# Performance work log

Measured on AMD Instinct MI355X. Metric: run time of the kernel, lower is better.

The kernel has to match this reference:

```python
import jax, jax.numpy as jnp
import numpy as np

B, N, C = 64, 256, 512
SHIFTS = (-1, 0, 1)
# torch.chunk(N, 3): ceil(256/3)=86 -> sizes [86, 86, 84]
CHUNK_SIZES = (86, 86, 84)
EPS = 1e-5


def _shift_pad(a, s):
    # shift along last axis (C) with zero padding, matching shift_with_padding
    if s == 0:
        return a
    if s > 0:
        return jnp.pad(a[..., :-s], ((0, 0), (0, 0), (s, 0)))
    s = -s
    return jnp.pad(a[..., s:], ((0, 0), (0, 0), (0, s)))


def setup_inputs() -> dict:
    key = jax.random.key(0)
    ks = jax.random.split(key, 16)
    w = lambda k, shape: (jax.random.normal(k, shape, jnp.float32) * 0.02)
    inp = {
        "x": jax.random.normal(ks[0], (B, N, C), jnp.float32),
        "ln_g": jnp.ones((C,), jnp.float32),
        "ln_b": jnp.zeros((C,), jnp.float32),
        "Ws": w(ks[1], (C, C)),
        "bs": jnp.zeros((C,), jnp.float32),
        "Wc": w(ks[2], (N, N, 3)),     # Conv1d weight [out=N, in=N, k=3]
        "bc": jnp.zeros((N,), jnp.float32),
        "We1": w(ks[3], (N, N // 8)),
        "be1": jnp.zeros((N // 8,), jnp.float32),
        "We2": w(ks[4], (N // 8, N)),
        "be2": jnp.zeros((N,), jnp.float32),
        "Wf1": w(ks[5], (C, 2 * C)),
        "bf1": jnp.zeros((2 * C,), jnp.float32),
        "Wf2": w(ks[6], (2 * C, C)),
        "bf2": jnp.zeros((C,), jnp.float32),
    }
    return inp


def reference(x, ln_g, ln_b, Ws, bs, Wc, bc, We1, be1, We2, be2, Wf1, bf1, Wf2, bf2):
    res = x
    # channel_mixer_S: LayerNorm over C, then Linear C->C + relu (dropout=0)
    mu = jnp.mean(x, axis=-1, keepdims=True)
    var = jnp.mean((x - mu) ** 2, axis=-1, keepdims=True)
    h = (x - mu) * jax.lax.rsqrt(var + EPS) * ln_g + ln_b
    h = jax.nn.relu(h @ Ws + bs)                      # [B, N, C]
    # channel_shift: chunk along N, shift each chunk along C with zero pad
    offs = np.cumsum((0,) + CHUNK_SIZES)
    chunks = [h[:, offs[i]:offs[i + 1], :] for i in range(3)]
    x_shift = jnp.concatenate([_shift_pad(c, s) for c, s in zip(chunks, SHIFTS)], axis=1)
    # channel_projection: Conv1d over C with N channels, k=3, pad=1
    x_shift = jax.lax.conv_general_dilated(
        x_shift, Wc, window_strides=(1,), padding=[(1, 1)],
        dimension_numbers=("NCH", "OIH", "NCH")) + bc[None, :, None]
    # SE gating
    se = jnp.mean(x_shift, axis=-1)                   # [B, N]
    ex = jax.nn.sigmoid(jax.nn.relu(se @ We1 + be1) @ We2 + be2)  # [B, N]
    z = x_shift * ex[:, :, None]
    # channel_mixer_F: C -> 2C (relu) -> C, residual
    z = jax.nn.relu(z @ Wf1 + bf1) @ Wf2 + bf2 + res
    return z
```

## Files before the change

### kernel.cpp

```cpp
#include <hip/hip_runtime.h>
#include <hip/hip_bf16.h>
#include <math.h>

#define BB 64
#define NN 256
#define CCH 512

typedef unsigned short u16;
typedef __attribute__((ext_vector_type(8))) short s16x8;
typedef __attribute__((ext_vector_type(4))) float f32x4;

#define AS1 __attribute__((address_space(1)))
#define AS3 __attribute__((address_space(3)))

static __device__ __forceinline__ float b2f(u16 u) {
    union { unsigned int i; float f; } x; x.i = ((unsigned int)u) << 16; return x.f;
}
static __device__ __forceinline__ u16 f2b(float f) {
    __hip_bfloat16 h = __float2bfloat16(f);
    union { __hip_bfloat16 h; u16 u; } x; x.h = h; return x.u;
}
static __device__ __forceinline__ void gll16(const void* g, void* l) {
    __builtin_amdgcn_global_load_lds((const AS1 unsigned int*)g,
                                     (AS3 unsigned int*)l, 16, 0, 0);
}

#define VM3  asm volatile("s_waitcnt vmcnt(3)" ::: "memory")
#define VM0  asm volatile("s_waitcnt vmcnt(0)" ::: "memory")
#define MEMB asm volatile("" ::: "memory")

__global__ __launch_bounds__(128) void ln_kernel(const float* __restrict__ x,
    const float* __restrict__ g, const float* __restrict__ bta,
    u16* __restrict__ out)
{
    int r = blockIdx.x;
    const float4* xr = (const float4*)(x + (size_t)r * CCH);
    float4 v = xr[threadIdx.x];
    float s  = v.x + v.y + v.z + v.w;
    float ss = v.x*v.x + v.y*v.y + v.z*v.z + v.w*v.w;
    #pragma unroll
    for (int o = 32; o > 0; o >>= 1) {
        s  += __shfl_down(s, o);
        ss += __shfl_down(ss, o);
    }
    __shared__ float red[4];
    int wid = threadIdx.x >> 6;
    if ((threadIdx.x & 63) == 0) { red[wid] = s; red[2 + wid] = ss; }
    __syncthreads();
    s  = red[0] + red[1];
    ss = red[2] + red[3];
    float mu  = s * (1.0f / CCH);
    float var = ss * (1.0f / CCH) - mu * mu;
    float rs  = rsqrtf(var + 1e-5f);
    float4 gv = ((const float4*)g)[threadIdx.x];
    float4 bv = ((const float4*)bta)[threadIdx.x];
    ushort4 o;
    o.x = f2b((v.x - mu) * rs * gv.x + bv.x);
    o.y = f2b((v.y - mu) * rs * gv.y + bv.y);
    o.z = f2b((v.z - mu) * rs * gv.z + bv.z);
    o.w = f2b((v.w - mu) * rs * gv.w + bv.w);
    ((ushort4*)(out + (size_t)r * CCH))[threadIdx.x] = o;
}

static __device__ __forceinline__ void wtc_body(const float* __restrict__ W,
    u16* __restrict__ Wt, int K, int N, int bx, int by, float* t )
{
    int n0 = bx * 32, k0 = by * 32;
    int tx = threadIdx.x & 31, ty = threadIdx.x >> 5;
    #pragma unroll
    for (int i = 0; i < 4; ++i)
        t[(ty + i * 8) * 33 + tx] = W[(size_t)(k0 + ty + i * 8) * N + n0 + tx];
    __syncthreads();
    #pragma unroll
    for (int i = 0; i < 4; ++i)
        Wt[(size_t)(n0 + ty + i * 8) * K + k0 + tx] = f2b(t[tx * 33 + ty + i * 8]);
}

__global__ __launch_bounds__(256) void prep_kernel(
    const float* __restrict__ Ws,  u16* __restrict__ Wst,
    const float* __restrict__ Wf1, u16* __restrict__ Wf1t,
    const float* __restrict__ Wf2, u16* __restrict__ Wf2t,
    const float* __restrict__ Wc,  u16* __restrict__ Wc3,
    u16* __restrict__ Hts, float* __restrict__ SEraw)
{
    __shared__ float t[32 * 33];
    int bid = blockIdx.x;
    if (bid < 256) {
        wtc_body(Ws, Wst, 512, 512, bid & 15, bid >> 4, t);
    } else if (bid < 768) {
        int idx = bid - 256;
        wtc_body(Wf1, Wf1t, 512, 1024, idx & 31, idx >> 5, t);
    } else if (bid < 1280) {
        int idx = bid - 768;
        wtc_body(Wf2, Wf2t, 1024, 512, idx & 15, idx >> 4, t);
    } else if (bid < 2048) {
        int idx = (bid - 1280) * 256 + threadIdx.x;
        int i = idx & 255;
        int o = (idx >> 8) & 255;
        int k = idx >> 16;
        Wc3[idx] = f2b(Wc[((size_t)o * NN + i) * 3 + k]);
    } else {
        int idx = (bid - 2048) * 256 + threadIdx.x;
        if (idx < 65536) {
            int b   = idx >> 10;
            int rem = idx & 1023;
            int rr  = rem >> 8;
            int r   = (rr & 1) + (rr >> 1) * 512;
            Hts[((size_t)b * 514 + r) * 256 + (rem & 255)] = 0;
        } else {
            SEraw[idx - 65536] = 0.0f;
        }
    }
}

template<int MODE>
__global__ __launch_bounds__(512, 1) void gemm_pipe(
    const u16* __restrict__ A, const u16* __restrict__ Bt,
    const float* __restrict__ bias, const float* __restrict__ scale,
    const float* __restrict__ res, void* __restrict__ outv,
    u16* __restrict__ auxout, float* __restrict__ SEraw)
{
    constexpr int NT = (MODE == 0) ? 8 : (MODE == 1) ? 8 : (MODE == 2) ? 16 : 12;
    constexpr int SA = (MODE == 2) ? 1024 : 512;
    constexpr int SB = (MODE == 2) ? 1024 : 512;
    constexpr int NOUT = (MODE == 1) ? 1024 : 512;

    __shared__ u16 Asm[2 * 2 * 256 * 32];
    __shared__ u16 Bsm[2 * 2 * 128 * 32];

    const int tid = threadIdx.x;
    const int l   = tid & 63;
    const int w   = tid >> 6;
    const int nwg = gridDim.x;
    const int work = (blockIdx.x & 7) * (nwg >> 3) + (blockIdx.x >> 3);

    int row0, col0, bidx = 0;
    if (MODE == 0)      { row0 = (work >> 7) * 256; col0 = (work & 127) * 128; }
    else if (MODE == 1) { row0 = (work >> 3) * 256; col0 = (work & 7) * 128; }
    else if (MODE == 2) { row0 = (work >> 2) * 256; col0 = (work & 3) * 128; }
    else                { row0 = 0; bidx = work >> 2; col0 = (work & 3) * 128; }

    const u16* Aab  = A + (size_t)row0 * SA;
    const u16* Bab  = Bt + (size_t)col0 * SB;
    const u16* HtsB = Bt + (size_t)bidx * 514 * 256;

    const int wm = (w >> 2) * 128;
    const int wn = (w & 3) * 32;
    const int fr = l & 15;
    const int fk = (l >> 4) * 8;

    const f32x4 zero = {0.0f, 0.0f, 0.0f, 0.0f};
    f32x4 acc[8][2];
    #pragma unroll
    for (int m = 0; m < 8; ++m) { acc[m][0] = zero; acc[m][1] = zero; }

    auto stageA = [&](int buf, int t1, int ks) {
        u16* ald = Asm + (buf * 2 + ks) * 8192 + w * 512;
        int s = w * 64 + l;
        if (MODE == 3) {
            const int kseg = t1 >> 2, kb = (t1 & 3) * 64 + ks * 32;
            gll16(A + kseg * 65536 + (s >> 2) * 256 + kb + (s & 3) * 8, ald);
            s += 512;
            gll16(A + kseg * 65536 + (s >> 2) * 256 + kb + (s & 3) * 8, ald + 4096);
        } else {
            const int kb = t1 * 64 + ks * 32;
            gll16(Aab + (size_t)(s >> 2) * SA + kb + (s & 3) * 8, ald);
            s += 512;
            gll16(Aab + (size_t)(s >> 2) * SA + kb + (s & 3) * 8, ald + 4096);
        }
    };
    auto stageB = [&](int buf, int t1, int ks) {
        u16* bld = Bsm + (buf * 2 + ks) * 4096 + w * 512;
        const int s = tid;
        if (MODE == 3) {
            const int kseg = t1 >> 2, kb = (t1 & 3) * 64 + ks * 32;
            gll16(HtsB + (size_t)(col0 + (s >> 2) + kseg) * 256 + kb + (s & 3) * 8, bld);
        } else {
            const int kb = t1 * 64 + ks * 32;
            gll16(Bab + (size_t)(s >> 2) * SB + kb + (s & 3) * 8, bld);
        }
    };

    stageA(0, 0, 0); stageB(0, 0, 0);
    stageA(0, 0, 1); stageB(0, 0, 1);

    int buf = 0;
    for (int t = 0; t < NT; ++t) {
        const bool more = (t + 1 < NT);
        #pragma unroll
        for (int ks = 0; ks < 2; ++ks) {
            if (ks == 0) { VM3; }
            else if (more) { VM3; } else { VM0; }
            __builtin_amdgcn_s_barrier();
            MEMB;
            s16x8 bf0 = *(const s16x8*)&Bsm[(buf * 2 + ks) * 4096 + (wn + 0 * 16 + fr) * 32 + fk];
            s16x8 bf1v = *(const s16x8*)&Bsm[(buf * 2 + ks) * 4096 + (wn + 1 * 16 + fr) * 32 + fk];
            s16x8 af[8];
            #pragma unroll
            for (int m = 0; m < 8; ++m)
                af[m] = *(const s16x8*)&Asm[(buf * 2 + ks) * 8192 + (wm + m * 16 + fr) * 32 + fk];
            if (more) { stageA(buf ^ 1, t + 1, ks); stageB(buf ^ 1, t + 1, ks); }
            __builtin_amdgcn_s_setprio(1);
            #pragma unroll
            for (int m = 0; m < 8; ++m) {
                acc[m][0] = __builtin_amdgcn_mfma_f32_16x16x32_bf16(af[m], bf0,  acc[m][0], 0, 0, 0);
                acc[m][1] = __builtin_amdgcn_mfma_f32_16x16x32_bf16(af[m], bf1v, acc[m][1], 0, 0, 0);
            }
            __builtin_amdgcn_s_setprio(0);
        }
        buf ^= 1;
    }

    if (MODE == 0) {
        #pragma unroll
        for (int m = 0; m < 8; ++m) {
            #pragma unroll
            for (int j = 0; j < 4; ++j) {
                const int c = row0 + wm + m * 16 + (l >> 4) * 4 + j;
                const float bsv = bias[c];
                #pragma unroll
                for (int n = 0; n < 2; ++n) {
                    const int gcol = col0 + wn + n * 16 + fr;
                    const int b  = gcol >> 8;
                    const int ni = gcol & 255;
                    const int s  = (ni < 86) ? -1 : (ni < 172 ? 0 : 1);
                    auxout[((size_t)b * 514 + c + 1 + s) * 256 + ni] =
                        f2b(fmaxf(acc[m][n][j] + bsv, 0.0f));
                }
            }
        }
    } else if (MODE == 1) {
        #pragma unroll
        for (int m = 0; m < 8; ++m) {
            #pragma unroll
            for (int j = 0; j < 4; ++j) {
                const int row = row0 + wm + m * 16 + (l >> 4) * 4 + j;
                const float sc = scale[row];
                #pragma unroll
                for (int n = 0; n < 2; ++n) {
                    const int col = col0 + wn + n * 16 + fr;
                    ((u16*)outv)[(size_t)row * NOUT + col] =
                        f2b(fmaxf(acc[m][n][j] * sc + bias[col], 0.0f));
                }
            }
        }
    } else if (MODE == 2) {
        #pragma unroll
        for (int m = 0; m < 8; ++m) {
            #pragma unroll
            for (int j = 0; j < 4; ++j) {
                const int row = row0 + wm + m * 16 + (l >> 4) * 4 + j;
                #pragma unroll
                for (int n = 0; n < 2; ++n) {
                    const int col = col0 + wn + n * 16 + fr;
                    ((float*)outv)[(size_t)row * NOUT + col] =
                        acc[m][n][j] + bias[col] + res[(size_t)row * NOUT + col];
                }
            }
        }
    } else {
        #pragma unroll
        for (int m = 0; m < 8; ++m) {
            #pragma unroll
            for (int j = 0; j < 4; ++j) {
                const int no = wm + m * 16 + (l >> 4) * 4 + j;
                const float bcv = bias[no];
                float p = 0.0f;
                #pragma unroll
                for (int n = 0; n < 2; ++n) {
                    const int c = col0 + wn + n * 16 + fr;
                    float v = acc[m][n][j];
                    auxout[((size_t)bidx * NN + no) * CCH + c] = f2b(v + bcv);
                    p += v;
                }
                p += __shfl_xor(p, 1);
                p += __shfl_xor(p, 2);
                p += __shfl_xor(p, 4);
                p += __shfl_xor(p, 8);
                if (fr == 0) atomicAdd(&SEraw[bidx * NN + no], p);
            }
        }
    }
}

__global__ __launch_bounds__(256) void semlp_kernel(const float* __restrict__ seraw,
    const float* __restrict__ bc,
    const float* __restrict__ We1, const float* __restrict__ be1,
    const float* __restrict__ We2, const float* __restrict__ be2,
    float* __restrict__ ex)
{
    __shared__ float sse[256];
    __shared__ float e1[32];
    int b = blockIdx.x, t = threadIdx.x;
    sse[t] = seraw[b * 256 + t] * (1.0f / CCH) + bc[t];
    __syncthreads();
    if (t < 32) {
        float a = be1[t];
        #pragma unroll 8
        for (int i = 0; i < 256; ++i) a += sse[i] * We1[i * 32 + t];
        e1[t] = fmaxf(a, 0.0f);
    }
    __syncthreads();
    float a = be2[t];
    #pragma unroll
    for (int j = 0; j < 32; ++j) a += e1[j] * We2[j * 256 + t];
    ex[b * 256 + t] = 1.0f / (1.0f + expf(-a));
}

extern "C" void kernel_launch(void* const* d_in, const int* in_sizes, int n_in,
                              void* d_out, int out_size, void* d_ws, size_t ws_size,
                              hipStream_t stream) {
    const float* x    = (const float*)d_in[0];
    const float* ln_g = (const float*)d_in[1];
    const float* ln_b = (const float*)d_in[2];
    const float* Ws   = (const float*)d_in[3];
    const float* bs   = (const float*)d_in[4];
    const float* Wc   = (const float*)d_in[5];
    const float* bc   = (const float*)d_in[6];
    const float* We1  = (const float*)d_in[7];
    const float* be1  = (const float*)d_in[8];
    const float* We2  = (const float*)d_in[9];
    const float* be2  = (const float*)d_in[10];
    const float* Wf1  = (const float*)d_in[11];
    const float* bf1  = (const float*)d_in[12];
    const float* Wf2  = (const float*)d_in[13];
    const float* bf2  = (const float*)d_in[14];
    float* out = (float*)d_out;
    char* w8   = (char*)d_ws;

    u16* XN  = (u16*)(w8);
    u16* Y   = XN;
    u16* Hts = (u16*)(w8 + (16u << 20));
    u16* T   = (u16*)(w8 + (16u << 20));
    char* tail = w8 + 50397184;
    float* SEraw = (float*)(tail);
    float* EX    = (float*)(tail + 65536);
    u16* Wst     = (u16*)(tail + 131072);
    u16* Wf1t    = (u16*)(tail + 655360);
    u16* Wf2t    = (u16*)(tail + 1703936);
    u16* Wc3     = (u16*)(tail + 2752512);

    prep_kernel<<<2368, 256, 0, stream>>>(Ws, Wst, Wf1, Wf1t, Wf2, Wf2t,
                                          Wc, Wc3, Hts, SEraw);
    ln_kernel<<<BB * NN, 128, 0, stream>>>(x, ln_g, ln_b, XN);
    gemm_pipe<0><<<256, 512, 0, stream>>>(Wst, XN, bs, nullptr, nullptr,
                                          nullptr, Hts, nullptr);
    gemm_pipe<3><<<256, 512, 0, stream>>>(Wc3, Hts, bc, nullptr, nullptr,
                                          nullptr, Y, SEraw);
    semlp_kernel<<<BB, 256, 0, stream>>>(SEraw, bc, We1, be1, We2, be2, EX);
    gemm_pipe<1><<<512, 512, 0, stream>>>(Y, Wf1t, bf1, EX, nullptr,
                                          T, nullptr, nullptr);
    gemm_pipe<2><<<256, 512, 0, stream>>>(T, Wf2t, bf2, nullptr, x,
                                          out, nullptr, nullptr);
}
```

Baseline: 134.7 us.

## Deepen GEMM pipeline to four LDS slots with XOR-swizzled K layout; wave-per-row LayerNorm

The GEMM main loop drops the double-buffered two-half-tile scheme and uses a 4-slot ring of 32-wide K steps, keeping three stages of global-to-LDS loads in flight (vmcnt 6). The K-chunk position inside each LDS row is XOR-swizzled on both the store side and the MFMA fragment read side, to cut LDS bank conflicts. LayerNorm now assigns one wave per row, four rows per block, and reduces with xor shuffles, removing the shared-memory reduction and the block barrier. The deeper prefetch trades one barrier per 32-K step for more outstanding loads.

```diff
diff --git a/kernel.cpp b/kernel.cpp
--- a/kernel.cpp
+++ b/kernel.cpp
@@ -25,41 +25,45 @@
                                      (AS3 unsigned int*)l, 16, 0, 0);
 }
 
+#define VM6  asm volatile("s_waitcnt vmcnt(6)" ::: "memory")
 #define VM3  asm volatile("s_waitcnt vmcnt(3)" ::: "memory")
 #define VM0  asm volatile("s_waitcnt vmcnt(0)" ::: "memory")
 #define MEMB asm volatile("" ::: "memory")
 
-__global__ __launch_bounds__(128) void ln_kernel(const float* __restrict__ x,
+__global__ __launch_bounds__(256) void ln_kernel(const float* __restrict__ x,
     const float* __restrict__ g, const float* __restrict__ bta,
     u16* __restrict__ out)
 {
-    int r = blockIdx.x;
+    const int l = threadIdx.x & 63;
+    const int r = blockIdx.x * 4 + (threadIdx.x >> 6);
     const float4* xr = (const float4*)(x + (size_t)r * CCH);
-    float4 v = xr[threadIdx.x];
-    float s  = v.x + v.y + v.z + v.w;
-    float ss = v.x*v.x + v.y*v.y + v.z*v.z + v.w*v.w;
+    float4 v1 = xr[l];
+    float4 v2 = xr[l + 64];
+    float s  = v1.x + v1.y + v1.z + v1.w + v2.x + v2.y + v2.z + v2.w;
+    float ss = v1.x*v1.x + v1.y*v1.y + v1.z*v1.z + v1.w*v1.w
+             + v2.x*v2.x + v2.y*v2.y + v2.z*v2.z + v2.w*v2.w;
     #pragma unroll
     for (int o = 32; o > 0; o >>= 1) {
-        s  += __shfl_down(s, o);
-        ss += __shfl_down(ss, o);
-    }
-    __shared__ float red[4];
-    int wid = threadIdx.x >> 6;
-    if ((threadIdx.x & 63) == 0) { red[wid] = s; red[2 + wid] = ss; }
-    __syncthreads();
-    s  = red[0] + red[1];
-    ss = red[2] + red[3];
+        s  += __shfl_xor(s, o);
+        ss += __shfl_xor(ss, o);
+    }
     float mu  = s * (1.0f / CCH);
     float var = ss * (1.0f / CCH) - mu * mu;
     float rs  = rsqrtf(var + 1e-5f);
-    float4 gv = ((const float4*)g)[threadIdx.x];
-    float4 bv = ((const float4*)bta)[threadIdx.x];
-    ushort4 o;
-    o.x = f2b((v.x - mu) * rs * gv.x + bv.x);
-    o.y = f2b((v.y - mu) * rs * gv.y + bv.y);
-    o.z = f2b((v.z - mu) * rs * gv.z + bv.z);
-    o.w = f2b((v.w - mu) * rs * gv.w + bv.w);
-    ((ushort4*)(out + (size_t)r * CCH))[threadIdx.x] = o;
+    float4 g1 = ((const float4*)g)[l],      g2 = ((const float4*)g)[l + 64];
+    float4 b1 = ((const float4*)bta)[l],    b2 = ((const float4*)bta)[l + 64];
+    ushort4 o1, o2;
+    o1.x = f2b((v1.x - mu) * rs * g1.x + b1.x);
+    o1.y = f2b((v1.y - mu) * rs * g1.y + b1.y);
+    o1.z = f2b((v1.z - mu) * rs * g1.z + b1.z);
+    o1.w = f2b((v1.w - mu) * rs * g1.w + b1.w);
+    o2.x = f2b((v2.x - mu) * rs * g2.x + b2.x);
+    o2.y = f2b((v2.y - mu) * rs * g2.y + b2.y);
+    o2.z = f2b((v2.z - mu) * rs * g2.z + b2.z);
+    o2.w = f2b((v2.w - mu) * rs * g2.w + b2.w);
+    ushort4* orow = (ushort4*)(out + (size_t)r * CCH);
+    orow[l]      = o1;
+    orow[l + 64] = o2;
 }
 
 static __device__ __forceinline__ void wtc_body(const float* __restrict__ W,
@@ -120,13 +124,13 @@
     const float* __restrict__ res, void* __restrict__ outv,
     u16* __restrict__ auxout, float* __restrict__ SEraw)
 {
-    constexpr int NT = (MODE == 0) ? 8 : (MODE == 1) ? 8 : (MODE == 2) ? 16 : 12;
+    constexpr int NK = (MODE == 2) ? 32 : (MODE == 3) ? 24 : 16;
     constexpr int SA = (MODE == 2) ? 1024 : 512;
     constexpr int SB = (MODE == 2) ? 1024 : 512;
     constexpr int NOUT = (MODE == 1) ? 1024 : 512;
 
-    __shared__ u16 Asm[2 * 2 * 256 * 32];
-    __shared__ u16 Bsm[2 * 2 * 128 * 32];
+    __shared__ u16 Asm[4 * 256 * 32];
+    __shared__ u16 Bsm[4 * 128 * 32];
 
     const int tid = threadIdx.x;
     const int l   = tid & 63;
@@ -147,68 +151,58 @@
     const int wm = (w >> 2) * 128;
     const int wn = (w & 3) * 32;
     const int fr = l & 15;
-    const int fk = (l >> 4) * 8;
+    const int q  = l >> 4;
+    const int kofs = ((q ^ ((l >> 1) & 3)) * 8);
 
     const f32x4 zero = {0.0f, 0.0f, 0.0f, 0.0f};
     f32x4 acc[8][2];
     #pragma unroll
     for (int m = 0; m < 8; ++m) { acc[m][0] = zero; acc[m][1] = zero; }
 
-    auto stageA = [&](int buf, int t1, int ks) {
-        u16* ald = Asm + (buf * 2 + ks) * 8192 + w * 512;
-        int s = w * 64 + l;
+    const int kc0 = ((tid & 3) ^ ((tid >> 3) & 3)) * 8;
+    const int srow = tid >> 2;
+
+    auto stage = [&](int u) {
+        const int slot = u & 3;
+        u16* ald = Asm + slot * 8192 + w * 512;
+        u16* bld = Bsm + slot * 4096 + w * 512;
         if (MODE == 3) {
-            const int kseg = t1 >> 2, kb = (t1 & 3) * 64 + ks * 32;
-            gll16(A + kseg * 65536 + (s >> 2) * 256 + kb + (s & 3) * 8, ald);
-            s += 512;
-            gll16(A + kseg * 65536 + (s >> 2) * 256 + kb + (s & 3) * 8, ald + 4096);
+            const int kseg = u >> 3, kb = (u & 7) * 32 + kc0;
+            gll16(A + kseg * 65536 + srow * 256 + kb, ald);
+            gll16(A + kseg * 65536 + (srow + 128) * 256 + kb, ald + 4096);
+            gll16(HtsB + (size_t)(col0 + srow + kseg) * 256 + kb, bld);
         } else {
-            const int kb = t1 * 64 + ks * 32;
-            gll16(Aab + (size_t)(s >> 2) * SA + kb + (s & 3) * 8, ald);
-            s += 512;
-            gll16(Aab + (size_t)(s >> 2) * SA + kb + (s & 3) * 8, ald + 4096);
+            const int kb = u * 32 + kc0;
+            gll16(Aab + (size_t)srow * SA + kb, ald);
+            gll16(Aab + (size_t)(srow + 128) * SA + kb, ald + 4096);
+            gll16(Bab + (size_t)srow * SB + kb, bld);
         }
     };
-    auto stageB = [&](int buf, int t1, int ks) {
-        u16* bld = Bsm + (buf * 2 + ks) * 4096 + w * 512;
-        const int s = tid;
-        if (MODE == 3) {
-            const int kseg = t1 >> 2, kb = (t1 & 3) * 64 + ks * 32;
-            gll16(HtsB + (size_t)(col0 + (s >> 2) + kseg) * 256 + kb + (s & 3) * 8, bld);
-        } else {
-            const int kb = t1 * 64 + ks * 32;
-            gll16(Bab + (size_t)(s >> 2) * SB + kb + (s & 3) * 8, bld);
-        }
-    };
-
-    stageA(0, 0, 0); stageB(0, 0, 0);
-    stageA(0, 0, 1); stageB(0, 0, 1);
-
-    int buf = 0;
-    for (int t = 0; t < NT; ++t) {
-        const bool more = (t + 1 < NT);
-        #pragma unroll
-        for (int ks = 0; ks < 2; ++ks) {
-            if (ks == 0) { VM3; }
-            else if (more) { VM3; } else { VM0; }
-            __builtin_amdgcn_s_barrier();
-            MEMB;
-            s16x8 bf0 = *(const s16x8*)&Bsm[(buf * 2 + ks) * 4096 + (wn + 0 * 16 + fr) * 32 + fk];
-            s16x8 bf1v = *(const s16x8*)&Bsm[(buf * 2 + ks) * 4096 + (wn + 1 * 16 + fr) * 32 + fk];
-            s16x8 af[8];
-            #pragma unroll
-            for (int m = 0; m < 8; ++m)
-                af[m] = *(const s16x8*)&Asm[(buf * 2 + ks) * 8192 + (wm + m * 16 + fr) * 32 + fk];
-            if (more) { stageA(buf ^ 1, t + 1, ks); stageB(buf ^ 1, t + 1, ks); }
-            __builtin_amdgcn_s_setprio(1);
-            #pragma unroll
-            for (int m = 0; m < 8; ++m) {
-                acc[m][0] = __builtin_amdgcn_mfma_f32_16x16x32_bf16(af[m], bf0,  acc[m][0], 0, 0, 0);
-                acc[m][1] = __builtin_amdgcn_mfma_f32_16x16x32_bf16(af[m], bf1v, acc[m][1], 0, 0, 0);
-            }
-            __builtin_amdgcn_s_setprio(0);
-        }
-        buf ^= 1;
+
+    stage(0); stage(1); stage(2);
+
+    for (int u = 0; u < NK; ++u) {
+        if (u < NK - 2)       { VM6; }
+        else if (u == NK - 2) { VM3; }
+        else                  { VM0; }
+        __builtin_amdgcn_s_barrier();
+        MEMB;
+        const int slot = u & 3;
+        s16x8 bf0  = *(const s16x8*)&Bsm[slot * 4096 + (wn + fr) * 32 + kofs];
+        s16x8 bf1v = *(const s16x8*)&Bsm[slot * 4096 + (wn + 16 + fr) * 32 + kofs];
+        s16x8 af[8];
+        #pragma unroll
+        for (int m = 0; m < 8; ++m)
+            af[m] = *(const s16x8*)&Asm[slot * 8192 + (wm + m * 16 + fr) * 32 + kofs];
+        if (u + 3 < NK) stage(u + 3);
+        __builtin_amdgcn_s_setprio(1);
+        #pragma unroll
+        for (int m = 0; m < 8; ++m) {
+            acc[m][0] = __builtin_amdgcn_mfma_f32_16x16x32_bf16(af[m], bf0,  acc[m][0], 0, 0, 0);
+            acc[m][1] = __builtin_amdgcn_mfma_f32_16x16x32_bf16(af[m], bf1v, acc[m][1], 0, 0, 0);
+        }
+        __builtin_amdgcn_s_setprio(0);
+        MEMB;
     }
 
     if (MODE == 0) {
@@ -342,7 +336,7 @@
 
     prep_kernel<<<2368, 256, 0, stream>>>(Ws, Wst, Wf1, Wf1t, Wf2, Wf2t,
                                           Wc, Wc3, Hts, SEraw);
-    ln_kernel<<<BB * NN, 128, 0, stream>>>(x, ln_g, ln_b, XN);
+    ln_kernel<<<BB * NN / 4, 256, 0, stream>>>(x, ln_g, ln_b, XN);
     gemm_pipe<0><<<256, 512, 0, stream>>>(Wst, XN, bs, nullptr, nullptr,
                                           nullptr, Hts, nullptr);
     gemm_pipe<3><<<256, 512, 0, stream>>>(Wc3, Hts, bc, nullptr, nullptr,
```

Result: faster. 129.5 us (-3.8%).
